# Kernel optimization log

Hardware: AMD Instinct MI355X
Metric: run time of the kernel (lower is better)

The kernel has to match this reference:

```python
import jax, jax.numpy as jnp
import numpy as np

N_SOTU, N_TAXON = 100000, 20000
E, EL = 800000, 200000
D_S, D_T, H = 256, 128, 256


def setup_inputs() -> dict:
    key = jax.random.key(0)
    ks = jax.random.split(key, 32)
    nrm = lambda k, shp: jax.random.normal(k, shp, jnp.float32) * 0.05
    inp = {}
    inp["x_sotu"] = nrm(ks[0], (N_SOTU, D_S))
    inp["x_taxon"] = nrm(ks[1], (N_TAXON, D_T))
    inp["edge_src"] = jax.random.randint(ks[2], (E,), 0, N_SOTU)   # sotu end
    inp["edge_dst"] = jax.random.randint(ks[3], (E,), 0, N_TAXON)  # taxon end
    inp["label_src"] = jax.random.randint(ks[4], (EL,), 0, N_SOTU)
    inp["label_dst"] = jax.random.randint(ks[5], (EL,), 0, N_TAXON)
    # conv1, edge type sotu->taxon
    inp["Wl1_st"] = nrm(ks[6], (H, D_S)); inp["bl1_st"] = jnp.zeros((H,), jnp.float32)
    inp["Wr1_st"] = nrm(ks[7], (H, D_T))
    # conv1, edge type taxon->sotu (reverse)
    inp["Wl1_ts"] = nrm(ks[8], (H, D_T)); inp["bl1_ts"] = jnp.zeros((H,), jnp.float32)
    inp["Wr1_ts"] = nrm(ks[9], (H, D_S))
    # conv2 (hidden -> hidden) per edge type
    inp["Wl2_st"] = nrm(ks[10], (H, H)); inp["bl2_st"] = jnp.zeros((H,), jnp.float32)
    inp["Wr2_st"] = nrm(ks[11], (H, H))
    inp["Wl2_ts"] = nrm(ks[12], (H, H)); inp["bl2_ts"] = jnp.zeros((H,), jnp.float32)
    inp["Wr2_ts"] = nrm(ks[13], (H, H))
    # final per-node-type linear (to_hetero duplicates Linear per node type)
    inp["Wlin_s"] = nrm(ks[14], (H, H)); inp["blin_s"] = jnp.zeros((H,), jnp.float32)
    inp["Wlin_t"] = nrm(ks[15], (H, H)); inp["blin_t"] = jnp.zeros((H,), jnp.float32)
    # edge decoder MLP
    inp["Wd1"] = nrm(ks[16], (H, 2 * H)); inp["bd1"] = jnp.zeros((H,), jnp.float32)
    inp["Wd2"] = nrm(ks[17], (1, H));     inp["bd2"] = jnp.zeros((1,), jnp.float32)
    return inp


def _sage(x_src, x_dst, src, dst, Wl, bl, Wr):
    """PyG SAGEConv (mean aggr): lin_l(mean of neighbor src feats) + lin_r(x_dst)."""
    n_dst = x_dst.shape[0]
    msum = jax.ops.segment_sum(x_src[src], dst, num_segments=n_dst)
    cnt = jax.ops.segment_sum(jnp.ones(src.shape, x_src.dtype), dst, num_segments=n_dst)
    m = msum / jnp.maximum(cnt, 1.0)[:, None]
    return m @ Wl.T + bl + x_dst @ Wr.T


def reference(x_sotu, x_taxon, edge_src, edge_dst, label_src, label_dst,
              Wl1_st, bl1_st, Wr1_st, Wl1_ts, bl1_ts, Wr1_ts,
              Wl2_st, bl2_st, Wr2_st, Wl2_ts, bl2_ts, Wr2_ts,
              Wlin_s, blin_s, Wlin_t, blin_t, Wd1, bd1, Wd2, bd2):
    # layer 1 (hetero SAGE, aggr='sum' over single incoming edge type per node type)
    h1_t = jax.nn.relu(_sage(x_sotu, x_taxon, edge_src, edge_dst, Wl1_st, bl1_st, Wr1_st))
    h1_s = jax.nn.relu(_sage(x_taxon, x_sotu, edge_dst, edge_src, Wl1_ts, bl1_ts, Wr1_ts))
    # layer 2
    h2_t = jax.nn.relu(_sage(h1_s, h1_t, edge_src, edge_dst, Wl2_st, bl2_st, Wr2_st))
    h2_s = jax.nn.relu(_sage(h1_t, h1_s, edge_dst, edge_src, Wl2_ts, bl2_ts, Wr2_ts))
    # per-node-type output projection
    z_s = h2_s @ Wlin_s.T + blin_s
    z_t = h2_t @ Wlin_t.T + blin_t
    # edge decoder: gather endpoint embeddings, concat, 2-layer MLP
    z = jnp.concatenate([z_s[label_src], z_t[label_dst]], axis=-1)  # [EL, 2H]
    h = jax.nn.relu(z @ Wd1.T + bd1)
    return (h @ Wd2.T + bd2).reshape(-1)  # [EL]
```

## Files before the change

kernel.cpp:

```cpp
#include <hip/hip_runtime.h>


constexpr int NS = 100000, NT = 20000;
constexpr int E_EDGES = 800000, EL_EDGES = 200000;
constexpr int DS = 256, DT = 128, H = 256;

constexpr int NB_T = 79, SH_T = 8, VB_T = 17;
constexpr int NB_S = 98, SH_S = 10, VB_S = 15;
constexpr int BIN_CAP = 96, CHUNK = 2048;

typedef __attribute__((ext_vector_type(8))) short short8;
typedef __attribute__((ext_vector_type(4))) float float4v;
typedef __attribute__((ext_vector_type(8))) _Float16 half8v;
typedef unsigned short ushort_t;

__device__ __forceinline__ float bf2f(unsigned int u) {
    union { unsigned int i; float f; } x; x.i = u << 16; return x.f;
}
__device__ __forceinline__ unsigned short f2bf(float f) {
    union { float f; unsigned int i; } x; x.f = f;
    unsigned int r = x.i + 0x7FFFu + ((x.i >> 16) & 1u);
    return (unsigned short)(r >> 16);
}

__global__ __launch_bounds__(512) void mgemm_kernel(
    const ushort_t* __restrict__ A1, const ushort_t* __restrict__ W1, int K1,
    const ushort_t* __restrict__ A2, const ushort_t* __restrict__ W2, int K2,
    const ushort_t* __restrict__ Add, const float* __restrict__ bias,
    void* __restrict__ Cout, int M, int flags)
{
    __shared__ ushort_t As[128][40];
    __shared__ ushort_t Bs[128][40];
    const int tid = threadIdx.x;

    const int nx = (M + 127) >> 7;
    const int nx8 = nx & ~7;
    const int bid = blockIdx.x;
    int rowblk, colblk;
    if (bid < nx8 * 2) {
        const int group = bid >> 4;
        const int xcd = bid & 7;
        const int half = (bid >> 3) & 1;
        rowblk = group * 8 + xcd;
        colblk = half;
    } else {
        const int r = bid - nx8 * 2;
        rowblk = nx8 + (r >> 1);
        colblk = r & 1;
    }
    const int row0 = rowblk * 128, col0 = colblk * 128;

    const int wave = tid >> 6, lane = tid & 63;
    const int wrow = (wave >> 1) * 32;
    const int wcol = (wave & 1) * 64;
    const int m16 = lane & 15, quad = lane >> 4;
    const int sr = tid >> 2;
    const int skc = (tid & 3) * 8;

    float4v acc[2][4];
#pragma unroll
    for (int i = 0; i < 2; i++)
#pragma unroll
        for (int j = 0; j < 4; j++) acc[i][j] = (float4v){0.f, 0.f, 0.f, 0.f};

#pragma unroll 1
    for (int pass = 0; pass < 2; pass++) {
        const ushort_t* A = pass ? A2 : A1;
        const ushort_t* W = pass ? W2 : W1;
        const int K = pass ? K2 : K1;
        if (!A) break;
        const int gra = row0 + sr;
        const bool oka = gra < M;
        const ushort_t* Ap = A + (size_t)gra * K + skc;
        const ushort_t* Wp = W + (size_t)(col0 + sr) * K + skc;

        uint4 a0 = make_uint4(0, 0, 0, 0);
        if (oka) a0 = *(const uint4*)Ap;
        uint4 b0 = *(const uint4*)Wp;

        for (int k0 = 0; k0 < K; k0 += 32) {
            __syncthreads();
            *(uint4*)&As[sr][skc] = a0;
            *(uint4*)&Bs[sr][skc] = b0;
            __syncthreads();
            if (k0 + 32 < K) {
                a0 = make_uint4(0, 0, 0, 0);
                if (oka) a0 = *(const uint4*)(Ap + k0 + 32);
                b0 = *(const uint4*)(Wp + k0 + 32);
            }
            short8 af[2], bf[4];
#pragma unroll
            for (int i = 0; i < 2; i++)
                af[i] = *(const short8*)&As[wrow + i * 16 + m16][quad * 8];
#pragma unroll
            for (int j = 0; j < 4; j++)
                bf[j] = *(const short8*)&Bs[wcol + j * 16 + m16][quad * 8];
#pragma unroll
            for (int i = 0; i < 2; i++)
#pragma unroll
                for (int j = 0; j < 4; j++)
                    acc[i][j] = __builtin_amdgcn_mfma_f32_16x16x32_bf16(
                        af[i], bf[j], acc[i][j], 0, 0, 0);
        }
    }

    const bool relu = flags & 1, f16out = flags & 2;
#pragma unroll
    for (int i = 0; i < 2; i++) {
        const int rbase = row0 + wrow + i * 16 + quad * 4;
#pragma unroll
        for (int r = 0; r < 4; r++) {
            const int row = rbase + r;
            if (row >= M) continue;
#pragma unroll
            for (int j = 0; j < 4; j++) {
                const int col = col0 + wcol + j * 16 + m16;
                float v = acc[i][j][r];
                if (Add) v += bf2f((unsigned int)Add[(size_t)row * 256 + col]);
                if (bias) v += bias[col];
                if (relu) v = fmaxf(v, 0.f);
                if (f16out) ((_Float16*)Cout)[(size_t)row * 256 + col] = (_Float16)v;
                else ((ushort_t*)Cout)[(size_t)row * 256 + col] = f2bf(v);
            }
        }
    }
}

struct CvtJobs {
    const float* src[14];
    ushort_t* dst[14];
    int n4[14];
    int cnt;
};

__global__ __launch_bounds__(256) void cvt_kernel(CvtJobs jb, int total4)
{
    int t = blockIdx.x * blockDim.x + threadIdx.x;
    if (t >= total4) return;
    int idx = t;
    for (int k = 0; k < jb.cnt; k++) {
        if (idx < jb.n4[k]) {
            float4 v = ((const float4*)jb.src[k])[idx];
            uint2 o;
            o.x = (unsigned int)f2bf(v.x) | ((unsigned int)f2bf(v.y) << 16);
            o.y = (unsigned int)f2bf(v.z) | ((unsigned int)f2bf(v.w) << 16);
            *(uint2*)(jb.dst[k] + (size_t)idx * 4) = o;
            return;
        }
        idx -= jb.n4[k];
    }
}

__global__ __launch_bounds__(256) void fold_kernel(
    const float* __restrict__ Wd1, const float* __restrict__ bd1,
    const float* __restrict__ Wlin_s, const float* __restrict__ blin_s,
    const float* __restrict__ Wlin_t, const float* __restrict__ blin_t,
    float* __restrict__ Wc_s, float* __restrict__ Wc_t,
    float* __restrict__ bu, float* __restrict__ bv)
{
    const int b = blockIdx.x, t = threadIdx.x;
    if (b < 256) {
        float s = 0.f;
        for (int k = 0; k < 256; k++) s += Wd1[b * 512 + k] * Wlin_s[k * 256 + t];
        Wc_s[b * 256 + t] = s;
    } else if (b < 512) {
        const int h = b - 256;
        float s = 0.f;
        for (int k = 0; k < 256; k++) s += Wd1[h * 512 + 256 + k] * Wlin_t[k * 256 + t];
        Wc_t[h * 256 + t] = s;
    } else {
        float su = 0.f, sv = 0.f;
        for (int k = 0; k < 256; k++) {
            su += Wd1[t * 512 + k] * blin_s[k];
            sv += Wd1[t * 512 + 256 + k] * blin_t[k];
        }
        bu[t] = bd1[t] + su;
        bv[t] = sv;
    }
}

__global__ void count_kernel(const int* __restrict__ src, const int* __restrict__ dst,
                             int* __restrict__ cnt_s, int* __restrict__ cnt_t, int E)
{
    int e = blockIdx.x * blockDim.x + threadIdx.x;
    if (e < E) {
        atomicAdd(&cnt_s[src[e]], 1);
        atomicAdd(&cnt_t[dst[e]], 1);
    }
}

__global__ __launch_bounds__(256) void psum_kernel(
    const int* __restrict__ cnt_s, const int* __restrict__ cnt_t,
    int* __restrict__ bsum_s, int* __restrict__ bsum_t, int nbS)
{
    const bool isS = (int)blockIdx.x < nbS;
    const int blk = isS ? blockIdx.x : blockIdx.x - nbS;
    const int N = isS ? NS : NT;
    const int* cnt = isS ? cnt_s : cnt_t;
    int* bsum = isS ? bsum_s : bsum_t;
    __shared__ int sdata[256];
    const int t = threadIdx.x;
    const int base = blk * 1024;
    int s = 0;
    for (int i = t; i < 1024; i += 256) {
        int idx = base + i;
        s += (idx < N) ? cnt[idx] : 0;
    }
    sdata[t] = s; __syncthreads();
    for (int off = 128; off > 0; off >>= 1) {
        if (t < off) sdata[t] += sdata[t + off];
        __syncthreads();
    }
    if (t == 0) bsum[blk] = sdata[0];
}

__global__ void sbsum_kernel(int* __restrict__ bsum_s, int* __restrict__ bsum_t,
                             int nbS, int nbT)
{
    if (threadIdx.x != 0) return;
    int* b = blockIdx.x ? bsum_t : bsum_s;
    int nb = blockIdx.x ? nbT : nbS;
    int run = 0;
    for (int i = 0; i < nb; i++) { int v = b[i]; b[i] = run; run += v; }
}

__global__ __launch_bounds__(256) void sblock_kernel(
    const int* __restrict__ cnt_s, const int* __restrict__ cnt_t,
    const int* __restrict__ bsum_s, const int* __restrict__ bsum_t,
    int* __restrict__ rowptr_s, int* __restrict__ rowptr_t, int nbS)
{
    const bool isS = (int)blockIdx.x < nbS;
    const int blk = isS ? blockIdx.x : blockIdx.x - nbS;
    const int N = isS ? NS : NT;
    const int* cnt = isS ? cnt_s : cnt_t;
    const int* bsum = isS ? bsum_s : bsum_t;
    int* rowptr = isS ? rowptr_s : rowptr_t;
    __shared__ int sc[256];
    const int t = threadIdx.x;
    const int base = blk * 1024 + t * 4;
    int v[4]; int s = 0;
#pragma unroll
    for (int j = 0; j < 4; j++) {
        int idx = base + j;
        v[j] = (idx < N) ? cnt[idx] : 0;
        s += v[j];
    }
    sc[t] = s; __syncthreads();
    for (int off = 1; off < 256; off <<= 1) {
        int add = (t >= off) ? sc[t - off] : 0;
        __syncthreads();
        sc[t] += add;
        __syncthreads();
    }
    int excl = sc[t] - s + bsum[blk];
#pragma unroll
    for (int j = 0; j < 4; j++) {
        int idx = base + j;
        if (idx < N) rowptr[idx] = excl;
        if (idx == N - 1) rowptr[N] = excl + v[j];
        excl += v[j];
    }
}

__global__ void binit_kernel(const int* __restrict__ rowptr_t,
                             const int* __restrict__ rowptr_s,
                             int* __restrict__ gcur_t, int* __restrict__ gcur_s)
{
    int t = threadIdx.x;
    if (t < NB_T) gcur_t[t] = rowptr_t[t << SH_T];
    if (t < NB_S) gcur_s[t] = rowptr_s[t << SH_S];
}

__global__ __launch_bounds__(256) void binA_kernel(
    const int* __restrict__ key, const int* __restrict__ val, int E,
    int nbins, int shift, int vbits,
    int* __restrict__ gcur, unsigned* __restrict__ stg)
{
    __shared__ unsigned bins[NB_S * BIN_CAP];
    __shared__ int lcnt[NB_S], gbase[NB_S];
    const int tid = threadIdx.x;
    const int base = blockIdx.x * CHUNK;
    for (int i = tid; i < nbins; i += 256) lcnt[i] = 0;
    __syncthreads();
    const unsigned lowmask = (1u << shift) - 1u;
#pragma unroll
    for (int k = 0; k < CHUNK / 256; k++) {
        int e = base + k * 256 + tid;
        if (e < E) {
            int kk = key[e];
            int b = kk >> shift;
            unsigned pk = (((unsigned)kk & lowmask) << vbits) | (unsigned)val[e];
            int c = atomicAdd(&lcnt[b], 1);
            if (c < BIN_CAP) bins[b * BIN_CAP + c] = pk;
            else { int p = atomicAdd(&gcur[b], 1); stg[p] = pk; }
        }
    }
    __syncthreads();
    if (tid < nbins) gbase[tid] = atomicAdd(&gcur[tid], min(lcnt[tid], BIN_CAP));
    __syncthreads();
    for (int b = 0; b < nbins; b++) {
        int c = min(lcnt[b], BIN_CAP);
        for (int i = tid; i < c; i += 256) stg[gbase[b] + i] = bins[b * BIN_CAP + i];
    }
}

__global__ __launch_bounds__(256) void binB_kernel(
    const unsigned* __restrict__ stg, const int* __restrict__ rowptr,
    int N, int node_per, int vbits, int* __restrict__ colout)
{
    __shared__ int cur[1024];
    const int tid = threadIdx.x;
    const int node0 = blockIdx.x * node_per;
    const int nn = min(node_per, N - node0);
    for (int i = tid; i < nn; i += 256) cur[i] = rowptr[node0 + i];
    const int estart = rowptr[node0];
    const int eend = rowptr[node0 + nn];
    __syncthreads();
    const unsigned vmask = (1u << vbits) - 1u;
    for (int i = estart + tid; i < eend; i += 256) {
        unsigned v = stg[i];
        int kl = (int)(v >> vbits);
        int pos = atomicAdd(&cur[kl], 1);
        colout[pos] = (int)(v & vmask);
    }
}

__global__ __launch_bounds__(256) void gather_mean_kernel(
    const ushort_t* __restrict__ X, const int* __restrict__ rowptr,
    const int* __restrict__ cnt, const int* __restrict__ col,
    ushort_t* __restrict__ out, int N)
{
    const int node = blockIdx.x * 8 + (threadIdx.x >> 5);
    const int c = (threadIdx.x & 31) * 8;
    if (node >= N) return;
    const int beg = rowptr[node];
    const int deg = cnt[node];
    const int end = beg + deg;
    float a[8] = {0, 0, 0, 0, 0, 0, 0, 0};
    float b[8] = {0, 0, 0, 0, 0, 0, 0, 0};
    int i = beg;
    for (; i + 1 < end; i += 2) {
        uint4 v = *(const uint4*)&X[(size_t)col[i] * 256 + c];
        uint4 w = *(const uint4*)&X[(size_t)col[i + 1] * 256 + c];
        a[0] += bf2f(v.x & 0xffff); a[1] += bf2f(v.x >> 16);
        a[2] += bf2f(v.y & 0xffff); a[3] += bf2f(v.y >> 16);
        a[4] += bf2f(v.z & 0xffff); a[5] += bf2f(v.z >> 16);
        a[6] += bf2f(v.w & 0xffff); a[7] += bf2f(v.w >> 16);
        b[0] += bf2f(w.x & 0xffff); b[1] += bf2f(w.x >> 16);
        b[2] += bf2f(w.y & 0xffff); b[3] += bf2f(w.y >> 16);
        b[4] += bf2f(w.z & 0xffff); b[5] += bf2f(w.z >> 16);
        b[6] += bf2f(w.w & 0xffff); b[7] += bf2f(w.w >> 16);
    }
    if (i < end) {
        uint4 v = *(const uint4*)&X[(size_t)col[i] * 256 + c];
        a[0] += bf2f(v.x & 0xffff); a[1] += bf2f(v.x >> 16);
        a[2] += bf2f(v.y & 0xffff); a[3] += bf2f(v.y >> 16);
        a[4] += bf2f(v.z & 0xffff); a[5] += bf2f(v.z >> 16);
        a[6] += bf2f(v.w & 0xffff); a[7] += bf2f(v.w >> 16);
    }
    float inv = 1.f / fmaxf((float)deg, 1.f);
    uint4 o;
    o.x = (unsigned int)f2bf((a[0] + b[0]) * inv) | ((unsigned int)f2bf((a[1] + b[1]) * inv) << 16);
    o.y = (unsigned int)f2bf((a[2] + b[2]) * inv) | ((unsigned int)f2bf((a[3] + b[3]) * inv) << 16);
    o.z = (unsigned int)f2bf((a[4] + b[4]) * inv) | ((unsigned int)f2bf((a[5] + b[5]) * inv) << 16);
    o.w = (unsigned int)f2bf((a[6] + b[6]) * inv) | ((unsigned int)f2bf((a[7] + b[7]) * inv) << 16);
    *(uint4*)&out[(size_t)node * 256 + c] = o;
}

__global__ __launch_bounds__(256) void edge_score_kernel(
    const _Float16* __restrict__ U, const _Float16* __restrict__ V,
    const int* __restrict__ ls, const int* __restrict__ ld,
    const float* __restrict__ Wd2, const float* __restrict__ bd2,
    float* __restrict__ out, int EL)
{
    const int l32 = threadIdx.x & 31;
    const int e = blockIdx.x * 8 + (threadIdx.x >> 5);
    if (e >= EL) return;
    const int c = l32 * 8;
    half8v u = *(const half8v*)&U[(size_t)ls[e] * 256 + c];
    half8v v = *(const half8v*)&V[(size_t)ld[e] * 256 + c];
    float4 w0 = *(const float4*)&Wd2[c];
    float4 w1 = *(const float4*)&Wd2[c + 4];
    float s = fmaxf((float)u[0] + (float)v[0], 0.f) * w0.x
            + fmaxf((float)u[1] + (float)v[1], 0.f) * w0.y
            + fmaxf((float)u[2] + (float)v[2], 0.f) * w0.z
            + fmaxf((float)u[3] + (float)v[3], 0.f) * w0.w
            + fmaxf((float)u[4] + (float)v[4], 0.f) * w1.x
            + fmaxf((float)u[5] + (float)v[5], 0.f) * w1.y
            + fmaxf((float)u[6] + (float)v[6], 0.f) * w1.z
            + fmaxf((float)u[7] + (float)v[7], 0.f) * w1.w;
#pragma unroll
    for (int m = 16; m >= 1; m >>= 1) s += __shfl_xor(s, m, 64);
    if (l32 == 0) out[e] = s + bd2[0];
}

extern "C" void kernel_launch(void* const* d_in, const int* in_sizes, int n_in,
                              void* d_out, int out_size, void* d_ws, size_t ws_size,
                              hipStream_t stream)
{
    const float* x_sotu  = (const float*)d_in[0];
    const float* x_taxon = (const float*)d_in[1];
    const int* edge_src  = (const int*)d_in[2];
    const int* edge_dst  = (const int*)d_in[3];
    const int* label_src = (const int*)d_in[4];
    const int* label_dst = (const int*)d_in[5];
    const float* Wl1_st = (const float*)d_in[6];
    const float* bl1_st = (const float*)d_in[7];
    const float* Wr1_st = (const float*)d_in[8];
    const float* Wl1_ts = (const float*)d_in[9];
    const float* bl1_ts = (const float*)d_in[10];
    const float* Wr1_ts = (const float*)d_in[11];
    const float* Wl2_st = (const float*)d_in[12];
    const float* bl2_st = (const float*)d_in[13];
    const float* Wr2_st = (const float*)d_in[14];
    const float* Wl2_ts = (const float*)d_in[15];
    const float* bl2_ts = (const float*)d_in[16];
    const float* Wr2_ts = (const float*)d_in[17];
    const float* Wlin_s = (const float*)d_in[18];
    const float* blin_s = (const float*)d_in[19];
    const float* Wlin_t = (const float*)d_in[20];
    const float* blin_t = (const float*)d_in[21];
    const float* Wd1 = (const float*)d_in[22];
    const float* bd1 = (const float*)d_in[23];
    const float* Wd2 = (const float*)d_in[24];
    const float* bd2 = (const float*)d_in[25];

    int* wi = (int*)d_ws;
    size_t io = 0;
    int* cnt_s   = wi + io; io += NS;
    int* cnt_t   = wi + io; io += NT;
    int* rowptr_s = wi + io; io += NS + 8;
    int* rowptr_t = wi + io; io += NT + 8;
    int* col_s   = wi + io; io += E_EDGES;
    int* col_t   = wi + io; io += E_EDGES;
    unsigned* stg_s = (unsigned*)(wi + io); io += E_EDGES;
    unsigned* stg_t = (unsigned*)(wi + io); io += E_EDGES;
    int* bsum_s  = wi + io; io += 128;
    int* bsum_t  = wi + io; io += 128;
    int* gcur_t  = wi + io; io += 128;
    int* gcur_s  = wi + io; io += 128;
    io = (io + 63) & ~(size_t)63;

    ushort_t* wb = (ushort_t*)(wi + io);
    size_t bo = 0;
    ushort_t* m_s  = wb + bo; bo += (size_t)NS * H;
    ushort_t* h1_s = wb + bo; bo += (size_t)NS * H;
    ushort_t* m_t  = wb + bo; bo += (size_t)NT * H;
    ushort_t* h1_t = wb + bo; bo += (size_t)NT * H;
    ushort_t* h2_s = wb + bo; bo += (size_t)NS * H;
    ushort_t* h2_t = wb + bo; bo += (size_t)NT * H;
    ushort_t* xs_b = wb + bo; bo += (size_t)NS * DS;
    ushort_t* xt_b = wb + bo; bo += (size_t)NT * DT;
    ushort_t* Pt   = wb + bo; bo += (size_t)NT * H;
    ushort_t* wb_l1st = wb + bo; bo += H * DS;
    ushort_t* wb_r1st = wb + bo; bo += H * DT;
    ushort_t* wb_l1ts = wb + bo; bo += H * DT;
    ushort_t* wb_r1ts = wb + bo; bo += H * DS;
    ushort_t* wb_l2st = wb + bo; bo += H * H;
    ushort_t* wb_r2st = wb + bo; bo += H * H;
    ushort_t* wb_l2ts = wb + bo; bo += H * H;
    ushort_t* wb_r2ts = wb + bo; bo += H * H;
    ushort_t* wcb_s   = wb + bo; bo += H * H;
    ushort_t* wcb_t   = wb + bo; bo += H * H;
    bo = (bo + 7) & ~(size_t)7;

    float* wf = (float*)(wb + bo);
    size_t fo = 0;
    float* Wc_s = wf + fo; fo += H * H;
    float* Wc_t = wf + fo; fo += H * H;
    float* bu   = wf + fo; fo += 256;
    float* bv   = wf + fo; fo += 256;

    _Float16* U = (_Float16*)m_s;
    _Float16* V = (_Float16*)m_t;

    const dim3 blk(256);
    const dim3 blk512(512);
    auto mg = [](int M) { return dim3(((M + 127) / 128) * 2); };
    const int nbS = (NS + 1023) / 1024;
    const int nbT = (NT + 1023) / 1024;
    const int nA = (E_EDGES + CHUNK - 1) / CHUNK;

    fold_kernel<<<513, blk, 0, stream>>>(Wd1, bd1, Wlin_s, blin_s, Wlin_t, blin_t,
                                         Wc_s, Wc_t, bu, bv);

    {
        CvtJobs jb; int c = 0, total4 = 0;
        auto addj = [&](const float* s, ushort_t* d, int n) {
            jb.src[c] = s; jb.dst[c] = d; jb.n4[c] = n / 4; total4 += n / 4; c++;
        };
        addj(x_sotu, xs_b, NS * DS);
        addj(x_taxon, xt_b, NT * DT);
        addj(Wl1_st, wb_l1st, H * DS);
        addj(Wr1_st, wb_r1st, H * DT);
        addj(Wl1_ts, wb_l1ts, H * DT);
        addj(Wr1_ts, wb_r1ts, H * DS);
        addj(Wl2_st, wb_l2st, H * H);
        addj(Wr2_st, wb_r2st, H * H);
        addj(Wl2_ts, wb_l2ts, H * H);
        addj(Wr2_ts, wb_r2ts, H * H);
        addj(Wc_s, wcb_s, H * H);
        addj(Wc_t, wcb_t, H * H);
        jb.cnt = c;
        cvt_kernel<<<(total4 + 255) / 256, blk, 0, stream>>>(jb, total4);
    }

    hipMemsetAsync(cnt_s, 0, (size_t)(NS + NT) * sizeof(int), stream);
    count_kernel<<<(E_EDGES + 255) / 256, blk, 0, stream>>>(edge_src, edge_dst,
                                                            cnt_s, cnt_t, E_EDGES);
    psum_kernel<<<nbS + nbT, blk, 0, stream>>>(cnt_s, cnt_t, bsum_s, bsum_t, nbS);
    sbsum_kernel<<<2, 64, 0, stream>>>(bsum_s, bsum_t, nbS, nbT);
    sblock_kernel<<<nbS + nbT, blk, 0, stream>>>(cnt_s, cnt_t, bsum_s, bsum_t,
                                                 rowptr_s, rowptr_t, nbS);
    binit_kernel<<<1, blk, 0, stream>>>(rowptr_t, rowptr_s, gcur_t, gcur_s);
    binA_kernel<<<nA, blk, 0, stream>>>(edge_dst, edge_src, E_EDGES,
                                        NB_T, SH_T, VB_T, gcur_t, stg_t);
    binA_kernel<<<nA, blk, 0, stream>>>(edge_src, edge_dst, E_EDGES,
                                        NB_S, SH_S, VB_S, gcur_s, stg_s);
    binB_kernel<<<NB_T, blk, 0, stream>>>(stg_t, rowptr_t, NT, 1 << SH_T, VB_T, col_t);
    binB_kernel<<<NB_S, blk, 0, stream>>>(stg_s, rowptr_s, NS, 1 << SH_S, VB_S, col_s);

    mgemm_kernel<<<mg(NT), blk512, 0, stream>>>(xt_b, wb_l1ts, DT, nullptr, nullptr, 0,
                                                nullptr, nullptr, Pt, NT, 0);
    gather_mean_kernel<<<(NT + 7) / 8, blk, 0, stream>>>(
        xs_b, rowptr_t, cnt_t, col_t, m_t, NT);
    gather_mean_kernel<<<(NS + 7) / 8, blk, 0, stream>>>(
        Pt, rowptr_s, cnt_s, col_s, m_s, NS);
    mgemm_kernel<<<mg(NT), blk512, 0, stream>>>(m_t, wb_l1st, H, xt_b, wb_r1st, DT,
                                                nullptr, bl1_st, h1_t, NT, 1);
    mgemm_kernel<<<mg(NS), blk512, 0, stream>>>(xs_b, wb_r1ts, DS, nullptr, nullptr, 0,
                                                m_s, bl1_ts, h1_s, NS, 1);

    mgemm_kernel<<<mg(NT), blk512, 0, stream>>>(h1_t, wb_l2ts, H, nullptr, nullptr, 0,
                                                nullptr, nullptr, Pt, NT, 0);
    gather_mean_kernel<<<(NT + 7) / 8, blk, 0, stream>>>(
        h1_s, rowptr_t, cnt_t, col_t, m_t, NT);
    gather_mean_kernel<<<(NS + 7) / 8, blk, 0, stream>>>(
        Pt, rowptr_s, cnt_s, col_s, m_s, NS);
    mgemm_kernel<<<mg(NT), blk512, 0, stream>>>(m_t, wb_l2st, H, h1_t, wb_r2st, H,
                                                nullptr, bl2_st, h2_t, NT, 1);
    mgemm_kernel<<<mg(NS), blk512, 0, stream>>>(h1_s, wb_r2ts, H, nullptr, nullptr, 0,
                                                m_s, bl2_ts, h2_s, NS, 1);

    mgemm_kernel<<<mg(NS), blk512, 0, stream>>>(h2_s, wcb_s, H, nullptr, nullptr, 0,
                                                nullptr, bu, U, NS, 2);
    mgemm_kernel<<<mg(NT), blk512, 0, stream>>>(h2_t, wcb_t, H, nullptr, nullptr, 0,
                                                nullptr, bv, V, NT, 2);
    edge_score_kernel<<<(EL_EDGES + 7) / 8, blk, 0, stream>>>(
        U, V, label_src, label_dst, Wd2, bd2, (float*)d_out, EL_EDGES);
}
```

Baseline: 904.6 us.

## Replace tiled GEMM with persistent weight-resident LDS GEMM kernel

Replaces the 128x128 K-chunked GEMM with a templated persistent kernel. It stages the entire 256xK weight matrix into LDS once, using XOR swizzling. Each wave then computes a full 32x256 output strip, streaming A fragments straight from global memory into registers with double buffering. The goal is to stop reloading weight tiles into LDS for every output block, and to cut barrier and launch-tile overhead. In exchange, the LDS footprint is large (up to 128 KB per block, which limits occupancy to one block per CU) and each wave holds 128 accumulator registers. Dual-operand GEMMs must also restage both weight matrices for every tile.

```diff
diff --git a/kernel.cpp b/kernel.cpp
--- a/kernel.cpp
+++ b/kernel.cpp
@@ -23,104 +23,144 @@
     return (unsigned short)(r >> 16);
 }
 
-__global__ __launch_bounds__(512) void mgemm_kernel(
-    const ushort_t* __restrict__ A1, const ushort_t* __restrict__ W1, int K1,
-    const ushort_t* __restrict__ A2, const ushort_t* __restrict__ W2, int K2,
+__device__ __forceinline__ float4v mfma16(short8 a, short8 b, float4v c) {
+    return __builtin_amdgcn_mfma_f32_16x16x32_bf16(a, b, c, 0, 0, 0);
+}
+
+
+template<int K>
+__device__ __forceinline__ void stageW(const ushort_t* __restrict__ W,
+                                       ushort_t* Bs, int tid)
+{
+    constexpr int CPC = K / 8;
+    constexpr int ROUNDS = 256 * CPC / 512;
+    uint4 v[ROUNDS];
+#pragma unroll
+    for (int r = 0; r < ROUNDS; ++r)
+        v[r] = *(const uint4*)(W + (size_t)(r * 512 + tid) * 8);
+#pragma unroll
+    for (int r = 0; r < ROUNDS; ++r) {
+        const int idx = r * 512 + tid;
+        const int col = idx / CPC;
+        const int c = idx & (CPC - 1);
+        *(uint4*)(Bs + (size_t)col * K + (size_t)((c ^ (col & 7)) << 3)) = v[r];
+    }
+}
+
+template<int K>
+__device__ __forceinline__ void computeK(const ushort_t* __restrict__ A,
+                                         const ushort_t* Bs, int rbase, int M,
+                                         int m16, int quad,
+                                         float4v (&acc)[2][16])
+{
+    constexpr int NKT = K / 32;
+    const ushort_t* Bsl = Bs + (size_t)m16 * K;
+    const int swz = m16 & 7;
+    const int r0 = min(rbase + m16, M - 1);
+    const int r1 = min(rbase + 16 + m16, M - 1);
+    const ushort_t* a0p = A + (size_t)r0 * K + quad * 8;
+    const ushort_t* a1p = A + (size_t)r1 * K + quad * 8;
+
+    short8 af0[2], af1[2];
+    af0[0] = *(const short8*)(a0p);
+    af0[1] = *(const short8*)(a1p);
+    af1[0] = *(const short8*)(a0p + 32);
+    af1[1] = *(const short8*)(a1p + 32);
+
+#pragma unroll
+    for (int kt = 0; kt < NKT; ++kt) {
+        const int koff = (((kt * 4 + quad) ^ swz) << 3);
+        const short8 a0 = (kt & 1) ? af1[0] : af0[0];
+        const short8 a1 = (kt & 1) ? af1[1] : af0[1];
+        short8 bfr[8];
+#pragma unroll
+        for (int j = 0; j < 8; ++j)
+            bfr[j] = *(const short8*)(Bsl + (size_t)j * (16 * K) + koff);
+#pragma unroll
+        for (int j = 0; j < 8; ++j) {
+            acc[0][j] = mfma16(a0, bfr[j], acc[0][j]);
+            acc[1][j] = mfma16(a1, bfr[j], acc[1][j]);
+        }
+#pragma unroll
+        for (int j = 0; j < 8; ++j)
+            bfr[j] = *(const short8*)(Bsl + (size_t)(j + 8) * (16 * K) + koff);
+#pragma unroll
+        for (int j = 0; j < 8; ++j) {
+            acc[0][j + 8] = mfma16(a0, bfr[j], acc[0][j + 8]);
+            acc[1][j + 8] = mfma16(a1, bfr[j], acc[1][j + 8]);
+        }
+        if (kt + 2 < NKT) {
+            if (kt & 1) {
+                af1[0] = *(const short8*)(a0p + (kt + 2) * 32);
+                af1[1] = *(const short8*)(a1p + (kt + 2) * 32);
+            } else {
+                af0[0] = *(const short8*)(a0p + (kt + 2) * 32);
+                af0[1] = *(const short8*)(a1p + (kt + 2) * 32);
+            }
+        }
+    }
+}
+
+template<int K1, int K2>
+__global__ __launch_bounds__(512, 2) void wgemm_kernel(
+    const ushort_t* __restrict__ A1, const ushort_t* __restrict__ W1,
+    const ushort_t* __restrict__ A2, const ushort_t* __restrict__ W2,
     const ushort_t* __restrict__ Add, const float* __restrict__ bias,
     void* __restrict__ Cout, int M, int flags)
 {
-    __shared__ ushort_t As[128][40];
-    __shared__ ushort_t Bs[128][40];
+    __shared__ ushort_t Bs[256 * K1];
     const int tid = threadIdx.x;
-
-    const int nx = (M + 127) >> 7;
-    const int nx8 = nx & ~7;
-    const int bid = blockIdx.x;
-    int rowblk, colblk;
-    if (bid < nx8 * 2) {
-        const int group = bid >> 4;
-        const int xcd = bid & 7;
-        const int half = (bid >> 3) & 1;
-        rowblk = group * 8 + xcd;
-        colblk = half;
-    } else {
-        const int r = bid - nx8 * 2;
-        rowblk = nx8 + (r >> 1);
-        colblk = r & 1;
-    }
-    const int row0 = rowblk * 128, col0 = colblk * 128;
-
     const int wave = tid >> 6, lane = tid & 63;
-    const int wrow = (wave >> 1) * 32;
-    const int wcol = (wave & 1) * 64;
     const int m16 = lane & 15, quad = lane >> 4;
-    const int sr = tid >> 2;
-    const int skc = (tid & 3) * 8;
-
-    float4v acc[2][4];
-#pragma unroll
-    for (int i = 0; i < 2; i++)
-#pragma unroll
-        for (int j = 0; j < 4; j++) acc[i][j] = (float4v){0.f, 0.f, 0.f, 0.f};
-
-#pragma unroll 1
-    for (int pass = 0; pass < 2; pass++) {
-        const ushort_t* A = pass ? A2 : A1;
-        const ushort_t* W = pass ? W2 : W1;
-        const int K = pass ? K2 : K1;
-        if (!A) break;
-        const int gra = row0 + sr;
-        const bool oka = gra < M;
-        const ushort_t* Ap = A + (size_t)gra * K + skc;
-        const ushort_t* Wp = W + (size_t)(col0 + sr) * K + skc;
-
-        uint4 a0 = make_uint4(0, 0, 0, 0);
-        if (oka) a0 = *(const uint4*)Ap;
-        uint4 b0 = *(const uint4*)Wp;
-
-        for (int k0 = 0; k0 < K; k0 += 32) {
+    const int ntiles = (M + 255) >> 8;
+    const bool relu = flags & 1, f16o = flags & 2;
+
+    stageW<K1>(W1, Bs, tid);
+    __syncthreads();
+
+    for (int tile = blockIdx.x; tile < ntiles; tile += gridDim.x) {
+        if constexpr (K2 > 0) {
+            if (tile != (int)blockIdx.x) {
+                __syncthreads();
+                stageW<K1>(W1, Bs, tid);
+                __syncthreads();
+            }
+        }
+        const int rbase = tile * 256 + wave * 32;
+
+        float4v acc[2][16];
+#pragma unroll
+        for (int i = 0; i < 2; ++i)
+#pragma unroll
+            for (int j = 0; j < 16; ++j) acc[i][j] = (float4v){0.f, 0.f, 0.f, 0.f};
+
+        computeK<K1>(A1, Bs, rbase, M, m16, quad, acc);
+
+        if constexpr (K2 > 0) {
             __syncthreads();
-            *(uint4*)&As[sr][skc] = a0;
-            *(uint4*)&Bs[sr][skc] = b0;
+            stageW<K2>(W2, Bs, tid);
             __syncthreads();
-            if (k0 + 32 < K) {
-                a0 = make_uint4(0, 0, 0, 0);
-                if (oka) a0 = *(const uint4*)(Ap + k0 + 32);
-                b0 = *(const uint4*)(Wp + k0 + 32);
-            }
-            short8 af[2], bf[4];
-#pragma unroll
-            for (int i = 0; i < 2; i++)
-                af[i] = *(const short8*)&As[wrow + i * 16 + m16][quad * 8];
-#pragma unroll
-            for (int j = 0; j < 4; j++)
-                bf[j] = *(const short8*)&Bs[wcol + j * 16 + m16][quad * 8];
-#pragma unroll
-            for (int i = 0; i < 2; i++)
-#pragma unroll
-                for (int j = 0; j < 4; j++)
-                    acc[i][j] = __builtin_amdgcn_mfma_f32_16x16x32_bf16(
-                        af[i], bf[j], acc[i][j], 0, 0, 0);
-        }
-    }
-
-    const bool relu = flags & 1, f16out = flags & 2;
-#pragma unroll
-    for (int i = 0; i < 2; i++) {
-        const int rbase = row0 + wrow + i * 16 + quad * 4;
-#pragma unroll
-        for (int r = 0; r < 4; r++) {
-            const int row = rbase + r;
-            if (row >= M) continue;
-#pragma unroll
-            for (int j = 0; j < 4; j++) {
-                const int col = col0 + wcol + j * 16 + m16;
-                float v = acc[i][j][r];
-                if (Add) v += bf2f((unsigned int)Add[(size_t)row * 256 + col]);
-                if (bias) v += bias[col];
-                if (relu) v = fmaxf(v, 0.f);
-                if (f16out) ((_Float16*)Cout)[(size_t)row * 256 + col] = (_Float16)v;
-                else ((ushort_t*)Cout)[(size_t)row * 256 + col] = f2bf(v);
+            computeK<K2>(A2, Bs, rbase, M, m16, quad, acc);
+        }
+
+#pragma unroll
+        for (int i = 0; i < 2; ++i) {
+            const int rb = rbase + i * 16 + quad * 4;
+#pragma unroll
+            for (int r = 0; r < 4; ++r) {
+                const int row = rb + r;
+                if (row >= M) continue;
+                const size_t ro = (size_t)row * 256;
+#pragma unroll
+                for (int j = 0; j < 16; ++j) {
+                    const int col = j * 16 + m16;
+                    float v = acc[i][j][r];
+                    if (Add) v += bf2f((unsigned int)Add[ro + col]);
+                    if (bias) v += bias[col];
+                    if (relu) v = fmaxf(v, 0.f);
+                    if (f16o) ((_Float16*)Cout)[ro + col] = (_Float16)v;
+                    else ((ushort_t*)Cout)[ro + col] = f2bf(v);
+                }
             }
         }
     }
@@ -475,8 +515,10 @@
     _Float16* V = (_Float16*)m_t;
 
     const dim3 blk(256);
-    const dim3 blk512(512);
-    auto mg = [](int M) { return dim3(((M + 127) / 128) * 2); };
+    auto wgrid = [](int M) {
+        int nt = (M + 255) >> 8;
+        return dim3(nt < 256 ? nt : 256);
+    };
     const int nbS = (NS + 1023) / 1024;
     const int nbT = (NT + 1023) / 1024;
     const int nA = (E_EDGES + CHUNK - 1) / CHUNK;
@@ -520,32 +562,32 @@
     binB_kernel<<<NB_T, blk, 0, stream>>>(stg_t, rowptr_t, NT, 1 << SH_T, VB_T, col_t);
     binB_kernel<<<NB_S, blk, 0, stream>>>(stg_s, rowptr_s, NS, 1 << SH_S, VB_S, col_s);
 
-    mgemm_kernel<<<mg(NT), blk512, 0, stream>>>(xt_b, wb_l1ts, DT, nullptr, nullptr, 0,
-                                                nullptr, nullptr, Pt, NT, 0);
+    wgemm_kernel<128, 0><<<wgrid(NT), 512, 0, stream>>>(
+        xt_b, wb_l1ts, nullptr, nullptr, nullptr, nullptr, Pt, NT, 0);
     gather_mean_kernel<<<(NT + 7) / 8, blk, 0, stream>>>(
         xs_b, rowptr_t, cnt_t, col_t, m_t, NT);
     gather_mean_kernel<<<(NS + 7) / 8, blk, 0, stream>>>(
         Pt, rowptr_s, cnt_s, col_s, m_s, NS);
-    mgemm_kernel<<<mg(NT), blk512, 0, stream>>>(m_t, wb_l1st, H, xt_b, wb_r1st, DT,
-                                                nullptr, bl1_st, h1_t, NT, 1);
-    mgemm_kernel<<<mg(NS), blk512, 0, stream>>>(xs_b, wb_r1ts, DS, nullptr, nullptr, 0,
-                                                m_s, bl1_ts, h1_s, NS, 1);
-
-    mgemm_kernel<<<mg(NT), blk512, 0, stream>>>(h1_t, wb_l2ts, H, nullptr, nullptr, 0,
-                                                nullptr, nullptr, Pt, NT, 0);
+    wgemm_kernel<256, 128><<<wgrid(NT), 512, 0, stream>>>(
+        m_t, wb_l1st, xt_b, wb_r1st, nullptr, bl1_st, h1_t, NT, 1);
+    wgemm_kernel<256, 0><<<wgrid(NS), 512, 0, stream>>>(
+        xs_b, wb_r1ts, nullptr, nullptr, m_s, bl1_ts, h1_s, NS, 1);
+
+    wgemm_kernel<256, 0><<<wgrid(NT), 512, 0, stream>>>(
+        h1_t, wb_l2ts, nullptr, nullptr, nullptr, nullptr, Pt, NT, 0);
     gather_mean_kernel<<<(NT + 7) / 8, blk, 0, stream>>>(
         h1_s, rowptr_t, cnt_t, col_t, m_t, NT);
     gather_mean_kernel<<<(NS + 7) / 8, blk, 0, stream>>>(
         Pt, rowptr_s, cnt_s, col_s, m_s, NS);
-    mgemm_kernel<<<mg(NT), blk512, 0, stream>>>(m_t, wb_l2st, H, h1_t, wb_r2st, H,
-                                                nullptr, bl2_st, h2_t, NT, 1);
-    mgemm_kernel<<<mg(NS), blk512, 0, stream>>>(h1_s, wb_r2ts, H, nullptr, nullptr, 0,
-                                                m_s, bl2_ts, h2_s, NS, 1);
-
-    mgemm_kernel<<<mg(NS), blk512, 0, stream>>>(h2_s, wcb_s, H, nullptr, nullptr, 0,
-                                                nullptr, bu, U, NS, 2);
-    mgemm_kernel<<<mg(NT), blk512, 0, stream>>>(h2_t, wcb_t, H, nullptr, nullptr, 0,
-                                                nullptr, bv, V, NT, 2);
+    wgemm_kernel<256, 256><<<wgrid(NT), 512, 0, stream>>>(
+        m_t, wb_l2st, h1_t, wb_r2st, nullptr, bl2_st, h2_t, NT, 1);
+    wgemm_kernel<256, 0><<<wgrid(NS), 512, 0, stream>>>(
+        h1_s, wb_r2ts, nullptr, nullptr, m_s, bl2_ts, h2_s, NS, 1);
+
+    wgemm_kernel<256, 0><<<wgrid(NS), 512, 0, stream>>>(
+        h2_s, wcb_s, nullptr, nullptr, nullptr, bu, U, NS, 2);
+    wgemm_kernel<256, 0><<<wgrid(NT), 512, 0, stream>>>(
+        h2_t, wcb_t, nullptr, nullptr, nullptr, bv, V, NT, 2);
     edge_score_kernel<<<(EL_EDGES + 7) / 8, blk, 0, stream>>>(
         U, V, label_src, label_dst, Wd2, bd2, (float*)d_out, EL_EDGES);
 }
```

New measurement: 1.196 ms. 1.32x slower.

## Co-schedule independent GEMM, gather and count stages in merged launches

Applied to the files above, without the earlier changes.

Independent stages are merged into single launches with block-index dispatch. Each layer's GEMM now runs alongside the neighbor-mean gather it does not depend on, the two final projection GEMMs share one launch, and the edge-count atomics run inside the bf16 conversion kernel. The aim is to cut the number of launches and fill each stage's tail with other work. The cost is that gather blocks now use 512 threads and carry the GEMM's shared-memory allocation, which can lower occupancy for the gather part.

```diff
diff --git a/kernel.cpp b/kernel.cpp
--- a/kernel.cpp
+++ b/kernel.cpp
@@ -23,19 +23,28 @@
     return (unsigned short)(r >> 16);
 }
 
-__global__ __launch_bounds__(512) void mgemm_kernel(
-    const ushort_t* __restrict__ A1, const ushort_t* __restrict__ W1, int K1,
-    const ushort_t* __restrict__ A2, const ushort_t* __restrict__ W2, int K2,
-    const ushort_t* __restrict__ Add, const float* __restrict__ bias,
-    void* __restrict__ Cout, int M, int flags)
+
+struct GemmJob {
+    const ushort_t* A1; const ushort_t* W1; int K1;
+    const ushort_t* A2; const ushort_t* W2; int K2;
+    const ushort_t* Add; const float* bias;
+    void* C; int M; int flags;
+};
+
+struct GatherJob {
+    const ushort_t* X; const int* rowptr; const int* cnt; const int* col;
+    ushort_t* out; int N;
+};
+
+__device__ __forceinline__ void gemm_body(const GemmJob& jb, int bid)
 {
     __shared__ ushort_t As[128][40];
     __shared__ ushort_t Bs[128][40];
     const int tid = threadIdx.x;
+    const int M = jb.M;
 
     const int nx = (M + 127) >> 7;
     const int nx8 = nx & ~7;
-    const int bid = blockIdx.x;
     int rowblk, colblk;
     if (bid < nx8 * 2) {
         const int group = bid >> 4;
@@ -65,9 +74,9 @@
 
 #pragma unroll 1
     for (int pass = 0; pass < 2; pass++) {
-        const ushort_t* A = pass ? A2 : A1;
-        const ushort_t* W = pass ? W2 : W1;
-        const int K = pass ? K2 : K1;
+        const ushort_t* A = pass ? jb.A2 : jb.A1;
+        const ushort_t* W = pass ? jb.W2 : jb.W1;
+        const int K = pass ? jb.K2 : jb.K1;
         if (!A) break;
         const int gra = row0 + sr;
         const bool oka = gra < M;
@@ -104,7 +113,7 @@
         }
     }
 
-    const bool relu = flags & 1, f16out = flags & 2;
+    const bool relu = jb.flags & 1, f16out = jb.flags & 2;
 #pragma unroll
     for (int i = 0; i < 2; i++) {
         const int rbase = row0 + wrow + i * 16 + quad * 4;
@@ -116,14 +125,76 @@
             for (int j = 0; j < 4; j++) {
                 const int col = col0 + wcol + j * 16 + m16;
                 float v = acc[i][j][r];
-                if (Add) v += bf2f((unsigned int)Add[(size_t)row * 256 + col]);
-                if (bias) v += bias[col];
+                if (jb.Add) v += bf2f((unsigned int)jb.Add[(size_t)row * 256 + col]);
+                if (jb.bias) v += jb.bias[col];
                 if (relu) v = fmaxf(v, 0.f);
-                if (f16out) ((_Float16*)Cout)[(size_t)row * 256 + col] = (_Float16)v;
-                else ((ushort_t*)Cout)[(size_t)row * 256 + col] = f2bf(v);
+                if (f16out) ((_Float16*)jb.C)[(size_t)row * 256 + col] = (_Float16)v;
+                else ((ushort_t*)jb.C)[(size_t)row * 256 + col] = f2bf(v);
             }
         }
     }
+}
+
+__device__ __forceinline__ void gather_body(const GatherJob& g, int gb)
+{
+    const int node = gb * 16 + (threadIdx.x >> 5);
+    const int c = (threadIdx.x & 31) * 8;
+    if (node >= g.N) return;
+    const int beg = g.rowptr[node];
+    const int deg = g.cnt[node];
+    const int end = beg + deg;
+    const ushort_t* __restrict__ X = g.X;
+    const int* __restrict__ col = g.col;
+    float a[8] = {0, 0, 0, 0, 0, 0, 0, 0};
+    float b[8] = {0, 0, 0, 0, 0, 0, 0, 0};
+    int i = beg;
+    for (; i + 1 < end; i += 2) {
+        uint4 v = *(const uint4*)&X[(size_t)col[i] * 256 + c];
+        uint4 w = *(const uint4*)&X[(size_t)col[i + 1] * 256 + c];
+        a[0] += bf2f(v.x & 0xffff); a[1] += bf2f(v.x >> 16);
+        a[2] += bf2f(v.y & 0xffff); a[3] += bf2f(v.y >> 16);
+        a[4] += bf2f(v.z & 0xffff); a[5] += bf2f(v.z >> 16);
+        a[6] += bf2f(v.w & 0xffff); a[7] += bf2f(v.w >> 16);
+        b[0] += bf2f(w.x & 0xffff); b[1] += bf2f(w.x >> 16);
+        b[2] += bf2f(w.y & 0xffff); b[3] += bf2f(w.y >> 16);
+        b[4] += bf2f(w.z & 0xffff); b[5] += bf2f(w.z >> 16);
+        b[6] += bf2f(w.w & 0xffff); b[7] += bf2f(w.w >> 16);
+    }
+    if (i < end) {
+        uint4 v = *(const uint4*)&X[(size_t)col[i] * 256 + c];
+        a[0] += bf2f(v.x & 0xffff); a[1] += bf2f(v.x >> 16);
+        a[2] += bf2f(v.y & 0xffff); a[3] += bf2f(v.y >> 16);
+        a[4] += bf2f(v.z & 0xffff); a[5] += bf2f(v.z >> 16);
+        a[6] += bf2f(v.w & 0xffff); a[7] += bf2f(v.w >> 16);
+    }
+    float inv = 1.f / fmaxf((float)deg, 1.f);
+    uint4 o;
+    o.x = (unsigned int)f2bf((a[0] + b[0]) * inv) | ((unsigned int)f2bf((a[1] + b[1]) * inv) << 16);
+    o.y = (unsigned int)f2bf((a[2] + b[2]) * inv) | ((unsigned int)f2bf((a[3] + b[3]) * inv) << 16);
+    o.z = (unsigned int)f2bf((a[4] + b[4]) * inv) | ((unsigned int)f2bf((a[5] + b[5]) * inv) << 16);
+    o.w = (unsigned int)f2bf((a[6] + b[6]) * inv) | ((unsigned int)f2bf((a[7] + b[7]) * inv) << 16);
+    *(uint4*)&g.out[(size_t)node * 256 + c] = o;
+}
+
+__global__ __launch_bounds__(512) void mgemm_kernel(GemmJob a)
+{
+    gemm_body(a, blockIdx.x);
+}
+
+__global__ __launch_bounds__(512) void gemm_gather_kernel(GemmJob a, int ablocks,
+                                                          GatherJob g)
+{
+    const int bid = blockIdx.x;
+    if (bid < ablocks) gemm_body(a, bid);
+    else gather_body(g, bid - ablocks);
+}
+
+__global__ __launch_bounds__(512) void gemm_gemm_kernel(GemmJob a, int ablocks,
+                                                        GemmJob b)
+{
+    const int bid = blockIdx.x;
+    if (bid < ablocks) gemm_body(a, bid);
+    else gemm_body(b, bid - ablocks);
 }
 
 struct CvtJobs {
@@ -133,8 +204,19 @@
     int cnt;
 };
 
-__global__ __launch_bounds__(256) void cvt_kernel(CvtJobs jb, int total4)
-{
+__global__ __launch_bounds__(256) void cvt_count_kernel(
+    CvtJobs jb, int total4, int cvtBlocks,
+    const int* __restrict__ src, const int* __restrict__ dst,
+    int* __restrict__ cnt_s, int* __restrict__ cnt_t, int E)
+{
+    if ((int)blockIdx.x >= cvtBlocks) {
+        int e = (blockIdx.x - cvtBlocks) * 256 + threadIdx.x;
+        if (e < E) {
+            atomicAdd(&cnt_s[src[e]], 1);
+            atomicAdd(&cnt_t[dst[e]], 1);
+        }
+        return;
+    }
     int t = blockIdx.x * blockDim.x + threadIdx.x;
     if (t >= total4) return;
     int idx = t;
@@ -179,16 +261,6 @@
     }
 }
 
-__global__ void count_kernel(const int* __restrict__ src, const int* __restrict__ dst,
-                             int* __restrict__ cnt_s, int* __restrict__ cnt_t, int E)
-{
-    int e = blockIdx.x * blockDim.x + threadIdx.x;
-    if (e < E) {
-        atomicAdd(&cnt_s[src[e]], 1);
-        atomicAdd(&cnt_t[dst[e]], 1);
-    }
-}
-
 __global__ __launch_bounds__(256) void psum_kernel(
     const int* __restrict__ cnt_s, const int* __restrict__ cnt_t,
     int* __restrict__ bsum_s, int* __restrict__ bsum_t, int nbS)
@@ -323,48 +395,6 @@
         int pos = atomicAdd(&cur[kl], 1);
         colout[pos] = (int)(v & vmask);
     }
-}
-
-__global__ __launch_bounds__(256) void gather_mean_kernel(
-    const ushort_t* __restrict__ X, const int* __restrict__ rowptr,
-    const int* __restrict__ cnt, const int* __restrict__ col,
-    ushort_t* __restrict__ out, int N)
-{
-    const int node = blockIdx.x * 8 + (threadIdx.x >> 5);
-    const int c = (threadIdx.x & 31) * 8;
-    if (node >= N) return;
-    const int beg = rowptr[node];
-    const int deg = cnt[node];
-    const int end = beg + deg;
-    float a[8] = {0, 0, 0, 0, 0, 0, 0, 0};
-    float b[8] = {0, 0, 0, 0, 0, 0, 0, 0};
-    int i = beg;
-    for (; i + 1 < end; i += 2) {
-        uint4 v = *(const uint4*)&X[(size_t)col[i] * 256 + c];
-        uint4 w = *(const uint4*)&X[(size_t)col[i + 1] * 256 + c];
-        a[0] += bf2f(v.x & 0xffff); a[1] += bf2f(v.x >> 16);
-        a[2] += bf2f(v.y & 0xffff); a[3] += bf2f(v.y >> 16);
-        a[4] += bf2f(v.z & 0xffff); a[5] += bf2f(v.z >> 16);
-        a[6] += bf2f(v.w & 0xffff); a[7] += bf2f(v.w >> 16);
-        b[0] += bf2f(w.x & 0xffff); b[1] += bf2f(w.x >> 16);
-        b[2] += bf2f(w.y & 0xffff); b[3] += bf2f(w.y >> 16);
-        b[4] += bf2f(w.z & 0xffff); b[5] += bf2f(w.z >> 16);
-        b[6] += bf2f(w.w & 0xffff); b[7] += bf2f(w.w >> 16);
-    }
-    if (i < end) {
-        uint4 v = *(const uint4*)&X[(size_t)col[i] * 256 + c];
-        a[0] += bf2f(v.x & 0xffff); a[1] += bf2f(v.x >> 16);
-        a[2] += bf2f(v.y & 0xffff); a[3] += bf2f(v.y >> 16);
-        a[4] += bf2f(v.z & 0xffff); a[5] += bf2f(v.z >> 16);
-        a[6] += bf2f(v.w & 0xffff); a[7] += bf2f(v.w >> 16);
-    }
-    float inv = 1.f / fmaxf((float)deg, 1.f);
-    uint4 o;
-    o.x = (unsigned int)f2bf((a[0] + b[0]) * inv) | ((unsigned int)f2bf((a[1] + b[1]) * inv) << 16);
-    o.y = (unsigned int)f2bf((a[2] + b[2]) * inv) | ((unsigned int)f2bf((a[3] + b[3]) * inv) << 16);
-    o.z = (unsigned int)f2bf((a[4] + b[4]) * inv) | ((unsigned int)f2bf((a[5] + b[5]) * inv) << 16);
-    o.w = (unsigned int)f2bf((a[6] + b[6]) * inv) | ((unsigned int)f2bf((a[7] + b[7]) * inv) << 16);
-    *(uint4*)&out[(size_t)node * 256 + c] = o;
 }
 
 __global__ __launch_bounds__(256) void edge_score_kernel(
@@ -476,7 +506,8 @@
 
     const dim3 blk(256);
     const dim3 blk512(512);
-    auto mg = [](int M) { return dim3(((M + 127) / 128) * 2); };
+    auto mgn = [](int M) { return ((M + 127) / 128) * 2; };
+    auto ggn = [](int N) { return (N + 15) / 16; };
     const int nbS = (NS + 1023) / 1024;
     const int nbT = (NT + 1023) / 1024;
     const int nA = (E_EDGES + CHUNK - 1) / CHUNK;
@@ -484,6 +515,7 @@
     fold_kernel<<<513, blk, 0, stream>>>(Wd1, bd1, Wlin_s, blin_s, Wlin_t, blin_t,
                                          Wc_s, Wc_t, bu, bv);
 
+    hipMemsetAsync(cnt_s, 0, (size_t)(NS + NT) * sizeof(int), stream);
     {
         CvtJobs jb; int c = 0, total4 = 0;
         auto addj = [&](const float* s, ushort_t* d, int n) {
@@ -502,12 +534,12 @@
         addj(Wc_s, wcb_s, H * H);
         addj(Wc_t, wcb_t, H * H);
         jb.cnt = c;
-        cvt_kernel<<<(total4 + 255) / 256, blk, 0, stream>>>(jb, total4);
-    }
-
-    hipMemsetAsync(cnt_s, 0, (size_t)(NS + NT) * sizeof(int), stream);
-    count_kernel<<<(E_EDGES + 255) / 256, blk, 0, stream>>>(edge_src, edge_dst,
-                                                            cnt_s, cnt_t, E_EDGES);
+        const int cvtBlocks = (total4 + 255) / 256;
+        const int cntBlocks = (E_EDGES + 255) / 256;
+        cvt_count_kernel<<<cvtBlocks + cntBlocks, blk, 0, stream>>>(
+            jb, total4, cvtBlocks, edge_src, edge_dst, cnt_s, cnt_t, E_EDGES);
+    }
+
     psum_kernel<<<nbS + nbT, blk, 0, stream>>>(cnt_s, cnt_t, bsum_s, bsum_t, nbS);
     sbsum_kernel<<<2, 64, 0, stream>>>(bsum_s, bsum_t, nbS, nbT);
     sblock_kernel<<<nbS + nbT, blk, 0, stream>>>(cnt_s, cnt_t, bsum_s, bsum_t,
@@ -520,32 +552,46 @@
     binB_kernel<<<NB_T, blk, 0, stream>>>(stg_t, rowptr_t, NT, 1 << SH_T, VB_T, col_t);
     binB_kernel<<<NB_S, blk, 0, stream>>>(stg_s, rowptr_s, NS, 1 << SH_S, VB_S, col_s);
 
-    mgemm_kernel<<<mg(NT), blk512, 0, stream>>>(xt_b, wb_l1ts, DT, nullptr, nullptr, 0,
-                                                nullptr, nullptr, Pt, NT, 0);
-    gather_mean_kernel<<<(NT + 7) / 8, blk, 0, stream>>>(
-        xs_b, rowptr_t, cnt_t, col_t, m_t, NT);
-    gather_mean_kernel<<<(NS + 7) / 8, blk, 0, stream>>>(
-        Pt, rowptr_s, cnt_s, col_s, m_s, NS);
-    mgemm_kernel<<<mg(NT), blk512, 0, stream>>>(m_t, wb_l1st, H, xt_b, wb_r1st, DT,
-                                                nullptr, bl1_st, h1_t, NT, 1);
-    mgemm_kernel<<<mg(NS), blk512, 0, stream>>>(xs_b, wb_r1ts, DS, nullptr, nullptr, 0,
-                                                m_s, bl1_ts, h1_s, NS, 1);
-
-    mgemm_kernel<<<mg(NT), blk512, 0, stream>>>(h1_t, wb_l2ts, H, nullptr, nullptr, 0,
-                                                nullptr, nullptr, Pt, NT, 0);
-    gather_mean_kernel<<<(NT + 7) / 8, blk, 0, stream>>>(
-        h1_s, rowptr_t, cnt_t, col_t, m_t, NT);
-    gather_mean_kernel<<<(NS + 7) / 8, blk, 0, stream>>>(
-        Pt, rowptr_s, cnt_s, col_s, m_s, NS);
-    mgemm_kernel<<<mg(NT), blk512, 0, stream>>>(m_t, wb_l2st, H, h1_t, wb_r2st, H,
-                                                nullptr, bl2_st, h2_t, NT, 1);
-    mgemm_kernel<<<mg(NS), blk512, 0, stream>>>(h1_s, wb_r2ts, H, nullptr, nullptr, 0,
-                                                m_s, bl2_ts, h2_s, NS, 1);
-
-    mgemm_kernel<<<mg(NS), blk512, 0, stream>>>(h2_s, wcb_s, H, nullptr, nullptr, 0,
-                                                nullptr, bu, U, NS, 2);
-    mgemm_kernel<<<mg(NT), blk512, 0, stream>>>(h2_t, wcb_t, H, nullptr, nullptr, 0,
-                                                nullptr, bv, V, NT, 2);
+    {
+        GemmJob a{xt_b, wb_l1ts, DT, nullptr, nullptr, 0, nullptr, nullptr, Pt, NT, 0};
+        GatherJob g{xs_b, rowptr_t, cnt_t, col_t, m_t, NT};
+        const int ab = mgn(NT);
+        gemm_gather_kernel<<<ab + ggn(NT), blk512, 0, stream>>>(a, ab, g);
+    }
+    {
+        GemmJob a{m_t, wb_l1st, H, xt_b, wb_r1st, DT, nullptr, bl1_st, h1_t, NT, 1};
+        GatherJob g{Pt, rowptr_s, cnt_s, col_s, m_s, NS};
+        const int ab = mgn(NT);
+        gemm_gather_kernel<<<ab + ggn(NS), blk512, 0, stream>>>(a, ab, g);
+    }
+    {
+        GemmJob a{xs_b, wb_r1ts, DS, nullptr, nullptr, 0, m_s, bl1_ts, h1_s, NS, 1};
+        mgemm_kernel<<<mgn(NS), blk512, 0, stream>>>(a);
+    }
+
+    {
+        GemmJob a{h1_t, wb_l2ts, H, nullptr, nullptr, 0, nullptr, nullptr, Pt, NT, 0};
+        GatherJob g{h1_s, rowptr_t, cnt_t, col_t, m_t, NT};
+        const int ab = mgn(NT);
+        gemm_gather_kernel<<<ab + ggn(NT), blk512, 0, stream>>>(a, ab, g);
+    }
+    {
+        GemmJob a{m_t, wb_l2st, H, h1_t, wb_r2st, H, nullptr, bl2_st, h2_t, NT, 1};
+        GatherJob g{Pt, rowptr_s, cnt_s, col_s, m_s, NS};
+        const int ab = mgn(NT);
+        gemm_gather_kernel<<<ab + ggn(NS), blk512, 0, stream>>>(a, ab, g);
+    }
+    {
+        GemmJob a{h1_s, wb_r2ts, H, nullptr, nullptr, 0, m_s, bl2_ts, h2_s, NS, 1};
+        mgemm_kernel<<<mgn(NS), blk512, 0, stream>>>(a);
+    }
+
+    {
+        GemmJob a{h2_s, wcb_s, H, nullptr, nullptr, 0, nullptr, bu, U, NS, 2};
+        GemmJob b{h2_t, wcb_t, H, nullptr, nullptr, 0, nullptr, bv, V, NT, 2};
+        const int ab = mgn(NS);
+        gemm_gemm_kernel<<<ab + mgn(NT), blk512, 0, stream>>>(a, ab, b);
+    }
     edge_score_kernel<<<(EL_EDGES + 7) / 8, blk, 0, stream>>>(
         U, V, label_src, label_dst, Wd2, bd2, (float*)d_out, EL_EDGES);
 }
```

New measurement: 914.5 us. No clear change (+1.1%).
